# Kernel optimization log

Hardware: AMD Instinct MI355X
Metric: run time of the kernel (lower is better)

Reference implementation:

```python
import jax, jax.numpy as jnp
import numpy as np

B, C, H, W = 2, 128, 48, 48
NUM_HEADS = 8


def dct_matrix(N):
    # Orthonormal DCT-II matrix: D[k, n] = s_k * cos(pi * (n + 0.5) * k / N)
    n = np.arange(N)
    D = np.cos(np.pi * (n[None, :] + 0.5) * n[:, None] / N) * np.sqrt(2.0 / N)
    D[0] *= 1.0 / np.sqrt(2.0)
    return jnp.asarray(D, dtype=jnp.float32)


def setup_inputs() -> dict:
    key = jax.random.key(0)
    ks = jax.random.split(key, 10)
    w_scale = 1.0 / np.sqrt(C)  # kaiming-ish init for 1x1 convs
    inp = {
        "freq_feat": jax.random.normal(ks[0], (B, C, H, W), dtype=jnp.float32),
        "spatial_feat": jax.random.normal(ks[1], (B, C, H, W), dtype=jnp.float32),
        "Wq": jax.random.normal(ks[2], (C, C), dtype=jnp.float32) * w_scale,
        "bq": jnp.zeros((C,), dtype=jnp.float32),
        "Wk": jax.random.normal(ks[3], (C, C), dtype=jnp.float32) * w_scale,
        "bk": jnp.zeros((C,), dtype=jnp.float32),
        "Wv": jax.random.normal(ks[4], (C, C), dtype=jnp.float32) * w_scale,
        "bv": jnp.zeros((C,), dtype=jnp.float32),
        "Wo": jax.random.normal(ks[5], (C, C), dtype=jnp.float32) * w_scale,
        "bo": jnp.zeros((C,), dtype=jnp.float32),
    }
    return inp


def _proj(x, Wm, b):
    # 1x1 conv == channel-mixing GEMM
    return jnp.einsum('oc,bchw->bohw', Wm, x) + b[None, :, None, None]


def reference(freq_feat, spatial_feat, Wq, bq, Wk, bk, Wv, bv, Wo, bo):
    b, c, h, w = freq_feat.shape
    nh = NUM_HEADS
    d = c // nh
    L = h * w

    # 2D orthonormal DCT-II of the spatial features
    DH = dct_matrix(h)
    DW = dct_matrix(w)
    spatial_freq = jnp.einsum('hm,bcmn,wn->bchw', DH, spatial_feat, DW)

    Q = _proj(freq_feat, Wq, bq)
    K = _proj(spatial_freq, Wk, bk)
    V = _proj(spatial_freq, Wv, bv)

    # (B, C, H, W) -> (B, nh, L, d)
    def to_heads(x):
        return x.reshape(b, nh, d, L).transpose(0, 1, 3, 2)

    Qh, Kh, Vh = to_heads(Q), to_heads(K), to_heads(V)

    scale = 1.0 / np.sqrt(d)
    scores = jnp.einsum('bhld,bhsd->bhls', Qh, Kh) * scale  # (B, nh, L, L)
    attn = jax.nn.softmax(scores, axis=-1)
    out = jnp.einsum('bhls,bhsd->bhld', attn, Vh)  # (B, nh, L, d)

    out = out.transpose(0, 1, 3, 2).reshape(b, c, h, w)
    return _proj(out, Wo, bo)
```

## Files before the change

kernel.cpp:

```cpp
#include <hip/hip_runtime.h>
#include <math.h>

#define L_TOT 2304
#define C_TOT 128
#define KSCALE 0.36067376022224085f

#if __has_builtin(__builtin_amdgcn_exp2f)
#define EXP2(x) __builtin_amdgcn_exp2f(x)
#else
#define EXP2(x) __expf(0.69314718055994531f * (x))
#endif

typedef float v4f  __attribute__((ext_vector_type(4)));
typedef __bf16 v8bf __attribute__((ext_vector_type(8)));
typedef __bf16 v4bf __attribute__((ext_vector_type(4)));

#define MFMA_16x16x32_BF16(A, B, C) __builtin_amdgcn_mfma_f32_16x16x32_bf16((A), (B), (C), 0, 0, 0)

__device__ __forceinline__ void async_cp16(const __bf16* g, __bf16* l){
  __builtin_amdgcn_global_load_lds((const __attribute__((address_space(1))) unsigned int*)g,
                                   (__attribute__((address_space(3))) unsigned int*)l,
                                   16, 0, 0);
}

#if __has_builtin(__builtin_amdgcn_permlane32_swap)
__device__ __forceinline__ void pl32swap(unsigned &a, unsigned &b){
  auto r = __builtin_amdgcn_permlane32_swap((int)a, (int)b, false, false);
  a = (unsigned)r[0]; b = (unsigned)r[1];
}
#else
__device__ __forceinline__ void pl32swap(unsigned &a, unsigned &b){
  asm volatile("v_permlane32_swap_b32 %0, %1" : "+v"(a), "+v"(b));
}
#endif
#if __has_builtin(__builtin_amdgcn_permlane16_swap)
__device__ __forceinline__ void pl16swap(unsigned &a, unsigned &b){
  auto r = __builtin_amdgcn_permlane16_swap((int)a, (int)b, false, false);
  a = (unsigned)r[0]; b = (unsigned)r[1];
}
#else
__device__ __forceinline__ void pl16swap(unsigned &a, unsigned &b){
  asm volatile("v_permlane16_swap_b32 %0, %1" : "+v"(a), "+v"(b));
}
#endif

template<int MODE>
__device__ __forceinline__ void mfma_proj(const float* __restrict__ W,
                                          const float* __restrict__ bias,
                                          const float* __restrict__ Xb,
                                          __bf16* __restrict__ Yh,
                                          float scale, float bscale,
                                          int n0, __bf16* Bhi, int tid){
  __bf16* Blo = Bhi + 4352;
  const int wave = tid >> 6, lane = tid & 63, qd = lane >> 4, cn = lane & 15;
  const int m0 = wave * 32;
  v8bf ahi[2][4], alo[2][4];
  #pragma unroll
  for (int rt = 0; rt < 2; rt++)
    #pragma unroll
    for (int ks = 0; ks < 4; ks++){
      const float* wp = W + (size_t)(m0 + rt * 16 + cn) * C_TOT + ks * 32 + qd * 8;
      float4 w0 = *(const float4*)wp;
      float4 w1 = *(const float4*)(wp + 4);
      float wv[8] = {w0.x, w0.y, w0.z, w0.w, w1.x, w1.y, w1.z, w1.w};
      #pragma unroll
      for (int j = 0; j < 8; j++){
        __bf16 h = (__bf16)wv[j];
        ahi[rt][ks][j] = h;
        alo[rt][ks][j] = (__bf16)(wv[j] - (float)h);
      }
    }
  {
    int k = tid >> 1, nh = tid & 1;
    const float* xp = Xb + (size_t)k * L_TOT + n0 + nh * 16;
    float4 x0 = *(const float4*)xp;
    float4 x1 = *(const float4*)(xp + 4);
    float4 x2 = *(const float4*)(xp + 8);
    float4 x3 = *(const float4*)(xp + 12);
    float xv[16] = {x0.x, x0.y, x0.z, x0.w, x1.x, x1.y, x1.z, x1.w,
                    x2.x, x2.y, x2.z, x2.w, x3.x, x3.y, x3.z, x3.w};
    #pragma unroll
    for (int i = 0; i < 16; i++){
      __bf16 h = (__bf16)xv[i];
      int row = nh * 16 + i;
      Bhi[row * 136 + k] = h;
      Blo[row * 136 + k] = (__bf16)(xv[i] - (float)h);
    }
  }
  __syncthreads();
  v4f acc[2][2];
  #pragma unroll
  for (int rt = 0; rt < 2; rt++)
    #pragma unroll
    for (int ct = 0; ct < 2; ct++) acc[rt][ct] = (v4f){0.f, 0.f, 0.f, 0.f};
  #pragma unroll
  for (int ks = 0; ks < 4; ks++){
    v8bf bhi[2], blo[2];
    #pragma unroll
    for (int ct = 0; ct < 2; ct++){
      bhi[ct] = *(const v8bf*)&Bhi[(ct * 16 + cn) * 136 + ks * 32 + qd * 8];
      blo[ct] = *(const v8bf*)&Blo[(ct * 16 + cn) * 136 + ks * 32 + qd * 8];
    }
    #pragma unroll
    for (int rt = 0; rt < 2; rt++)
      #pragma unroll
      for (int ct = 0; ct < 2; ct++){
        acc[rt][ct] = MFMA_16x16x32_BF16(ahi[rt][ks], bhi[ct], acc[rt][ct]);
        acc[rt][ct] = MFMA_16x16x32_BF16(ahi[rt][ks], blo[ct], acc[rt][ct]);
        acc[rt][ct] = MFMA_16x16x32_BF16(alo[rt][ks], bhi[ct], acc[rt][ct]);
      }
  }
  #pragma unroll
  for (int rt = 0; rt < 2; rt++){
    float bv[4];
    #pragma unroll
    for (int r = 0; r < 4; r++) bv[r] = bias[m0 + rt * 16 + qd * 4 + r] * bscale;
    #pragma unroll
    for (int ct = 0; ct < 2; ct++){
      int col = n0 + ct * 16 + cn;
      if (MODE == 1){
        v4bf kk;
        #pragma unroll
        for (int r = 0; r < 4; r++) kk[r] = (__bf16)((acc[rt][ct][r] + bv[r]) * scale);
        *(v4bf*)&Yh[(size_t)col * C_TOT + m0 + rt * 16 + qd * 4] = kk;
      } else {
        #pragma unroll
        for (int r = 0; r < 4; r++)
          Yh[(size_t)(m0 + rt * 16 + qd * 4 + r) * L_TOT + col] = (__bf16)(acc[rt][ct][r] + bv[r]);
      }
    }
  }
}

__global__ __launch_bounds__(256) void k_q_dct(
    const float* __restrict__ freq, const float* __restrict__ spat,
    const float* __restrict__ Wq, const float* __restrict__ bq,
    __bf16* __restrict__ QT, float* __restrict__ SF){
  __shared__ __align__(16) unsigned char smraw[34560];
  int tid = threadIdx.x;
  if (blockIdx.x < 144){
    int idx = blockIdx.x;
    int b = idx / 72, n0 = (idx % 72) * 32;
    size_t off = (size_t)b * C_TOT * L_TOT;
    mfma_proj<1>(Wq, bq, freq + off, QT + (size_t)b * L_TOT * C_TOT, 1.0f, 1.0f, n0, (__bf16*)smraw, tid);
    return;
  }
  int img = blockIdx.x - 144;
  __bf16* Xhi = (__bf16*)smraw;
  __bf16* Xlo = Xhi + 3456;
  __bf16* Dm  = Xhi + 6912;
  __bf16* Thi = Xhi + 10368;
  __bf16* Tlo = Xhi + 13824;
  const float* src = spat + (size_t)img * 2304;
  for (int i = tid; i < 8640; i += 256) ((unsigned int*)smraw)[i] = 0u;
  __syncthreads();
  for (int i = tid; i < 2304; i += 256){
    int a = i / 48, n = i - a * 48;
    int m = ((2 * n + 1) * a) % 192;
    float v = cosf(0.032724923474893679f * (float)m) * 0.204124145231931508f;
    if (a == 0) v *= 0.707106781186547524f;
    Dm[a * 72 + n] = (__bf16)v;
  }
  for (int i = tid; i < 2304; i += 256){
    int mm = i / 48, n = i - mm * 48;
    float v = src[i];
    __bf16 h = (__bf16)v;
    Xhi[mm * 72 + n] = h;
    Xlo[mm * 72 + n] = (__bf16)(v - (float)h);
  }
  __syncthreads();
  int wave = tid >> 6, lane = tid & 63, qd = lane >> 4, cn = lane & 15;
  for (int t = wave; t < 9; t += 4){
    int mi = t / 3, wi = t - mi * 3;
    v8bf ah0 = *(const v8bf*)&Xhi[(mi * 16 + cn) * 72 + qd * 8];
    v8bf ah1 = *(const v8bf*)&Xhi[(mi * 16 + cn) * 72 + 32 + qd * 8];
    v8bf al0 = *(const v8bf*)&Xlo[(mi * 16 + cn) * 72 + qd * 8];
    v8bf al1 = *(const v8bf*)&Xlo[(mi * 16 + cn) * 72 + 32 + qd * 8];
    v8bf b0 = *(const v8bf*)&Dm[(wi * 16 + cn) * 72 + qd * 8];
    v8bf b1 = *(const v8bf*)&Dm[(wi * 16 + cn) * 72 + 32 + qd * 8];
    v4f acc = (v4f){0.f, 0.f, 0.f, 0.f};
    acc = MFMA_16x16x32_BF16(ah0, b0, acc);
    acc = MFMA_16x16x32_BF16(ah1, b1, acc);
    acc = MFMA_16x16x32_BF16(al0, b0, acc);
    acc = MFMA_16x16x32_BF16(al1, b1, acc);
    v4bf th, tl;
    #pragma unroll
    for (int r = 0; r < 4; r++){
      __bf16 h = (__bf16)acc[r];
      th[r] = h;
      tl[r] = (__bf16)(acc[r] - (float)h);
    }
    *(v4bf*)&Thi[(wi * 16 + cn) * 72 + mi * 16 + qd * 4] = th;
    *(v4bf*)&Tlo[(wi * 16 + cn) * 72 + mi * 16 + qd * 4] = tl;
  }
  __syncthreads();
  float* dst = SF + (size_t)img * 2304;
  for (int t = wave; t < 9; t += 4){
    int hi_ = t / 3, wi = t - hi_ * 3;
    v8bf a0 = *(const v8bf*)&Dm[(hi_ * 16 + cn) * 72 + qd * 8];
    v8bf a1 = *(const v8bf*)&Dm[(hi_ * 16 + cn) * 72 + 32 + qd * 8];
    v8bf bh0 = *(const v8bf*)&Thi[(wi * 16 + cn) * 72 + qd * 8];
    v8bf bh1 = *(const v8bf*)&Thi[(wi * 16 + cn) * 72 + 32 + qd * 8];
    v8bf bl0 = *(const v8bf*)&Tlo[(wi * 16 + cn) * 72 + qd * 8];
    v8bf bl1 = *(const v8bf*)&Tlo[(wi * 16 + cn) * 72 + 32 + qd * 8];
    v4f acc = (v4f){0.f, 0.f, 0.f, 0.f};
    acc = MFMA_16x16x32_BF16(a0, bh0, acc);
    acc = MFMA_16x16x32_BF16(a1, bh1, acc);
    acc = MFMA_16x16x32_BF16(a0, bl0, acc);
    acc = MFMA_16x16x32_BF16(a1, bl1, acc);
    int w = wi * 16 + cn;
    #pragma unroll
    for (int r = 0; r < 4; r++)
      dst[(size_t)(hi_ * 16 + qd * 4 + r) * 48 + w] = acc[r];
  }
}

__global__ __launch_bounds__(256) void k_kv(
    const float* __restrict__ SF,
    const float* __restrict__ Wk, const float* __restrict__ bk,
    const float* __restrict__ Wv, const float* __restrict__ bv,
    __bf16* __restrict__ KT, __bf16* __restrict__ Vg){
  __shared__ __align__(16) unsigned char smraw[17408];
  int job = blockIdx.x / 144;
  int idx = blockIdx.x % 144;
  int b = idx / 72, n0 = (idx % 72) * 32;
  size_t off = (size_t)b * C_TOT * L_TOT;
  if (job == 0)
    mfma_proj<1>(Wk, bk, SF + off, KT + (size_t)b * L_TOT * C_TOT, KSCALE, 1.0f, n0, (__bf16*)smraw, threadIdx.x);
  else
    mfma_proj<2>(Wv, bv, SF + off, Vg + off, 1.0f, 1.0f, n0, (__bf16*)smraw, threadIdx.x);
}

__global__ __launch_bounds__(256) void k_attn(const __bf16* __restrict__ QT,
                                              const __bf16* __restrict__ KT,
                                              const __bf16* __restrict__ V,
                                              __bf16* __restrict__ AO){
  const int L = L_TOT;
  int bh = blockIdx.y;
  int b = bh >> 3, h = bh & 7;
  int c0 = h * 16;
  const __bf16* QTb = QT + (size_t)b * L * C_TOT;
  const __bf16* KTb = KT + (size_t)b * L * C_TOT;
  const __bf16* Vb  = V  + ((size_t)b * C_TOT + c0) * L;
  int tid = threadIdx.x;
  int wave = tid >> 6, lane = tid & 63;
  int qd = lane >> 4, cn = lane & 15;
  int l0 = blockIdx.x * 48;

  __shared__ __align__(16) __bf16 smem[8192 + 8192];
  __bf16* Kt = smem;
  __bf16* Vs = smem + 8192;

  v8bf qf[3];
  #pragma unroll
  for (int t = 0; t < 3; t++){
    #pragma unroll
    for (int j = 0; j < 8; j++) qf[t][j] = (__bf16)0.0f;
  }
  if (qd < 2){
    #pragma unroll
    for (int t = 0; t < 3; t++)
      qf[t] = *(const v8bf*)&QTb[(size_t)(l0 + t * 16 + cn) * C_TOT + c0 + qd * 8];
  }

  v4f acc[3];
  float den[3] = {0.f, 0.f, 0.f};
  #pragma unroll
  for (int t = 0; t < 3; t++) acc[t] = (v4f){0.f, 0.f, 0.f, 0.f};

  for (int ch = 0; ch < 5; ch++){
    int s0 = ch * 512;
    int cnt = (ch == 4) ? 256 : 512;
    __syncthreads();
    {
      int per = (cnt >> 5) >> 2;
      for (int jj = 0; jj < per; jj++){
        int j = wave * per + jj;
        int s = j * 32 + (lane >> 1);
        async_cp16(KTb + (size_t)(s0 + s) * C_TOT + c0 + (lane & 1) * 8,
                   Kt + j * 512);
      }
      if (cnt == 512){
        #pragma unroll
        for (int jj = 0; jj < 4; jj++){
          int d = wave * 4 + jj;
          async_cp16(Vb + (size_t)d * L + s0 + ((lane ^ (d & 7)) << 3),
                     Vs + d * 512);
        }
      } else {
        int d = tid >> 4, og = tid & 15;
        const __bf16* gp = Vb + (size_t)d * L + s0 + og * 16;
        v8bf v0 = *(const v8bf*)gp;
        v8bf v1 = *(const v8bf*)(gp + 8);
        int pd = d & 7;
        *(v8bf*)&Vs[d * 512 + (((og * 2)     ^ pd) << 3)] = v0;
        *(v8bf*)&Vs[d * 512 + (((og * 2 + 1) ^ pd) << 3)] = v1;
      }
    }
    __syncthreads();

    int nsu = cnt >> 7;
    int wbase = wave * (cnt >> 2);
    for (int su = 0; su < nsu; su++){
      int sb = wbase + su * 32;
      v8bf a0, a1;
      #pragma unroll
      for (int j = 0; j < 8; j++){ a0[j] = (__bf16)0.0f; a1[j] = (__bf16)0.0f; }
      if (qd < 2){
        a0 = *(const v8bf*)&Kt[(sb + cn) * 16 + qd * 8];
        a1 = *(const v8bf*)&Kt[(sb + 16 + cn) * 16 + qd * 8];
      }
      int jv = sb >> 3;
      v8bf vf = *(const v8bf*)&Vs[cn * 512 + (((jv + qd) ^ (cn & 7)) << 3)];
      #pragma unroll
      for (int t = 0; t < 3; t++){
        v4f z = {0.f, 0.f, 0.f, 0.f};
        v4f st0 = MFMA_16x16x32_BF16(a0, qf[t], z);
        v4f st1 = MFMA_16x16x32_BF16(a1, qf[t], z);
        float p0[4], p1[4];
        #pragma unroll
        for (int i = 0; i < 4; i++){
          p0[i] = EXP2(st0[i]); den[t] += p0[i];
          p1[i] = EXP2(st1[i]); den[t] += p1[i];
        }
        v4bf cc0, cc1;
        #pragma unroll
        for (int i = 0; i < 4; i++){ cc0[i] = (__bf16)p0[i]; cc1[i] = (__bf16)p1[i]; }
        unsigned U0 = ((unsigned*)&cc0)[0], U1 = ((unsigned*)&cc0)[1];
        unsigned U2 = ((unsigned*)&cc1)[0], U3 = ((unsigned*)&cc1)[1];
        pl32swap(U0, U2); pl32swap(U1, U3);
        pl16swap(U0, U2); pl16swap(U1, U3);
        v8bf pf;
        ((unsigned*)&pf)[0] = U0; ((unsigned*)&pf)[1] = U1;
        ((unsigned*)&pf)[2] = U2; ((unsigned*)&pf)[3] = U3;
        acc[t] = MFMA_16x16x32_BF16(vf, pf, acc[t]);
      }
    }
  }

  __syncthreads();
  float* redA = (float*)smem;
  float* redD = (float*)smem + 3072;
  #pragma unroll
  for (int t = 0; t < 3; t++){
    *(v4f*)&redA[((wave * 3 + t) * 64 + lane) * 4] = acc[t];
    redD[(wave * 3 + t) * 64 + lane] = den[t];
  }
  __syncthreads();
  if (wave < 3){
    int t = wave;
    v4f a = (v4f){0.f, 0.f, 0.f, 0.f};
    float dn = 0.f;
    #pragma unroll
    for (int w2 = 0; w2 < 4; w2++){
      v4f xx = *(const v4f*)&redA[((w2 * 3 + t) * 64 + lane) * 4];
      a[0] += xx[0]; a[1] += xx[1]; a[2] += xx[2]; a[3] += xx[3];
      dn += redD[(w2 * 3 + t) * 64 + lane];
    }
    dn += __shfl_xor(dn, 16);
    dn += __shfl_xor(dn, 32);
    float inv = 1.0f / dn;
    __bf16* Ao = AO + ((size_t)b * C_TOT + c0) * L;
    #pragma unroll
    for (int r2 = 0; r2 < 4; r2++)
      Ao[(size_t)(qd * 4 + r2) * L + l0 + t * 16 + cn] = (__bf16)(a[r2] * inv);
  }
}

__global__ __launch_bounds__(256) void k_oproj(const __bf16* __restrict__ AO,
                                               const float* __restrict__ Wo, const float* __restrict__ bo,
                                               float* __restrict__ out){
  __shared__ __align__(16) __bf16 Bs[32 * 136];
  int b = blockIdx.y, n0 = blockIdx.x * 32;
  int tid = threadIdx.x;
  const int wave = tid >> 6, lane = tid & 63, qd = lane >> 4, cn = lane & 15;
  const int m0 = wave * 32;
  v8bf ahi[2][4], alo[2][4];
  #pragma unroll
  for (int rt = 0; rt < 2; rt++)
    #pragma unroll
    for (int ks = 0; ks < 4; ks++){
      const float* wp = Wo + (size_t)(m0 + rt * 16 + cn) * C_TOT + ks * 32 + qd * 8;
      float4 w0 = *(const float4*)wp;
      float4 w1 = *(const float4*)(wp + 4);
      float wv[8] = {w0.x, w0.y, w0.z, w0.w, w1.x, w1.y, w1.z, w1.w};
      #pragma unroll
      for (int j = 0; j < 8; j++){
        __bf16 h = (__bf16)wv[j];
        ahi[rt][ks][j] = h;
        alo[rt][ks][j] = (__bf16)(wv[j] - (float)h);
      }
    }
  {
    int k = tid >> 1, nh = tid & 1;
    const __bf16* src = AO + ((size_t)b * C_TOT + k) * L_TOT + n0 + nh * 16;
    v8bf x0 = *(const v8bf*)src;
    v8bf x1 = *(const v8bf*)(src + 8);
    #pragma unroll
    for (int i = 0; i < 8; i++){
      Bs[(nh * 16 + i) * 136 + k] = x0[i];
      Bs[(nh * 16 + 8 + i) * 136 + k] = x1[i];
    }
  }
  __syncthreads();
  v4f acc[2][2];
  #pragma unroll
  for (int rt = 0; rt < 2; rt++)
    #pragma unroll
    for (int ct = 0; ct < 2; ct++) acc[rt][ct] = (v4f){0.f, 0.f, 0.f, 0.f};
  #pragma unroll
  for (int ks = 0; ks < 4; ks++){
    v8bf bf[2];
    #pragma unroll
    for (int ct = 0; ct < 2; ct++)
      bf[ct] = *(const v8bf*)&Bs[(ct * 16 + cn) * 136 + ks * 32 + qd * 8];
    #pragma unroll
    for (int rt = 0; rt < 2; rt++)
      #pragma unroll
      for (int ct = 0; ct < 2; ct++){
        acc[rt][ct] = MFMA_16x16x32_BF16(ahi[rt][ks], bf[ct], acc[rt][ct]);
        acc[rt][ct] = MFMA_16x16x32_BF16(alo[rt][ks], bf[ct], acc[rt][ct]);
      }
  }
  float* ob = out + (size_t)b * C_TOT * L_TOT;
  #pragma unroll
  for (int rt = 0; rt < 2; rt++){
    float bv[4];
    #pragma unroll
    for (int r = 0; r < 4; r++) bv[r] = bo[m0 + rt * 16 + qd * 4 + r];
    #pragma unroll
    for (int ct = 0; ct < 2; ct++){
      int col = n0 + ct * 16 + cn;
      #pragma unroll
      for (int r = 0; r < 4; r++)
        ob[(size_t)(m0 + rt * 16 + qd * 4 + r) * L_TOT + col] = acc[rt][ct][r] + bv[r];
    }
  }
}

extern "C" void kernel_launch(void* const* d_in, const int* in_sizes, int n_in,
                              void* d_out, int out_size, void* d_ws, size_t ws_size,
                              hipStream_t stream){
  const float* freq = (const float*)d_in[0];
  const float* spat = (const float*)d_in[1];
  const float* Wq = (const float*)d_in[2]; const float* bq = (const float*)d_in[3];
  const float* Wk = (const float*)d_in[4]; const float* bk = (const float*)d_in[5];
  const float* Wv = (const float*)d_in[6]; const float* bv = (const float*)d_in[7];
  const float* Wo = (const float*)d_in[8]; const float* bo = (const float*)d_in[9];
  __bf16* base = (__bf16*)d_ws;

  __bf16* QTg = base;
  __bf16* KTg = base + 589824;
  __bf16* Vg  = base + 1179648;
  __bf16* AOg = base + 1769472;
  float*  SFg = (float*)(base + 2359296);
  float* out = (float*)d_out;

  k_q_dct<<<dim3(400), dim3(256), 0, stream>>>(freq, spat, Wq, bq, QTg, SFg);
  k_kv<<<dim3(288), dim3(256), 0, stream>>>(SFg, Wk, bk, Wv, bv, KTg, Vg);
  k_attn<<<dim3(48, 16), dim3(256), 0, stream>>>(QTg, KTg, Vg, AOg);
  k_oproj<<<dim3(72, 2), dim3(256), 0, stream>>>(AOg, Wo, bo, out);
}
```

Baseline: 115.8 us.

## Double-buffer per-wave K/V async staging in attention and halve projection tiles

The attention kernel replaces its block-wide five-chunk K/V staging loop, which needed two __syncthreads per chunk, with per-wave double-buffered async copies. Each wave prefetches the next 64-key slice while computing on the current one, synchronised only by vmcnt waits, so load latency should overlap with MFMA work. Separately, the Q, K/V and output projection kernels move to 16-column tiles, doubling the block count to fill more CUs at the cost of reloading and splitting the weights more often. The per-wave buffers mean each wave handles only its own key range, and the split-precision weight setup is repeated in twice as many blocks.

```diff
diff --git a/kernel.cpp b/kernel.cpp
--- a/kernel.cpp
+++ b/kernel.cpp
@@ -44,14 +44,14 @@
 }
 #endif
 
-template<int MODE>
+template<int MODE, int NT>
 __device__ __forceinline__ void mfma_proj(const float* __restrict__ W,
                                           const float* __restrict__ bias,
                                           const float* __restrict__ Xb,
                                           __bf16* __restrict__ Yh,
                                           float scale, float bscale,
                                           int n0, __bf16* Bhi, int tid){
-  __bf16* Blo = Bhi + 4352;
+  __bf16* Blo = Bhi + NT * 2176;
   const int wave = tid >> 6, lane = tid & 63, qd = lane >> 4, cn = lane & 15;
   const int m0 = wave * 32;
   v8bf ahi[2][4], alo[2][4];
@@ -70,7 +70,7 @@
         alo[rt][ks][j] = (__bf16)(wv[j] - (float)h);
       }
     }
-  {
+  if (NT == 2){
     int k = tid >> 1, nh = tid & 1;
     const float* xp = Xb + (size_t)k * L_TOT + n0 + nh * 16;
     float4 x0 = *(const float4*)xp;
@@ -86,25 +86,38 @@
       Bhi[row * 136 + k] = h;
       Blo[row * 136 + k] = (__bf16)(xv[i] - (float)h);
     }
-  }
-  __syncthreads();
-  v4f acc[2][2];
+  } else {
+    int k = tid >> 1, half = tid & 1;
+    const float* xp = Xb + (size_t)k * L_TOT + n0 + half * 8;
+    float4 x0 = *(const float4*)xp;
+    float4 x1 = *(const float4*)(xp + 4);
+    float xv[8] = {x0.x, x0.y, x0.z, x0.w, x1.x, x1.y, x1.z, x1.w};
+    #pragma unroll
+    for (int i = 0; i < 8; i++){
+      __bf16 h = (__bf16)xv[i];
+      int row = half * 8 + i;
+      Bhi[row * 136 + k] = h;
+      Blo[row * 136 + k] = (__bf16)(xv[i] - (float)h);
+    }
+  }
+  __syncthreads();
+  v4f acc[2][NT];
   #pragma unroll
   for (int rt = 0; rt < 2; rt++)
     #pragma unroll
-    for (int ct = 0; ct < 2; ct++) acc[rt][ct] = (v4f){0.f, 0.f, 0.f, 0.f};
+    for (int ct = 0; ct < NT; ct++) acc[rt][ct] = (v4f){0.f, 0.f, 0.f, 0.f};
   #pragma unroll
   for (int ks = 0; ks < 4; ks++){
-    v8bf bhi[2], blo[2];
-    #pragma unroll
-    for (int ct = 0; ct < 2; ct++){
+    v8bf bhi[NT], blo[NT];
+    #pragma unroll
+    for (int ct = 0; ct < NT; ct++){
       bhi[ct] = *(const v8bf*)&Bhi[(ct * 16 + cn) * 136 + ks * 32 + qd * 8];
       blo[ct] = *(const v8bf*)&Blo[(ct * 16 + cn) * 136 + ks * 32 + qd * 8];
     }
     #pragma unroll
     for (int rt = 0; rt < 2; rt++)
       #pragma unroll
-      for (int ct = 0; ct < 2; ct++){
+      for (int ct = 0; ct < NT; ct++){
         acc[rt][ct] = MFMA_16x16x32_BF16(ahi[rt][ks], bhi[ct], acc[rt][ct]);
         acc[rt][ct] = MFMA_16x16x32_BF16(ahi[rt][ks], blo[ct], acc[rt][ct]);
         acc[rt][ct] = MFMA_16x16x32_BF16(alo[rt][ks], bhi[ct], acc[rt][ct]);
@@ -116,7 +129,7 @@
     #pragma unroll
     for (int r = 0; r < 4; r++) bv[r] = bias[m0 + rt * 16 + qd * 4 + r] * bscale;
     #pragma unroll
-    for (int ct = 0; ct < 2; ct++){
+    for (int ct = 0; ct < NT; ct++){
       int col = n0 + ct * 16 + cn;
       if (MODE == 1){
         v4bf kk;
@@ -138,14 +151,14 @@
     __bf16* __restrict__ QT, float* __restrict__ SF){
   __shared__ __align__(16) unsigned char smraw[34560];
   int tid = threadIdx.x;
-  if (blockIdx.x < 144){
+  if (blockIdx.x < 288){
     int idx = blockIdx.x;
-    int b = idx / 72, n0 = (idx % 72) * 32;
+    int b = idx / 144, n0 = (idx % 144) * 16;
     size_t off = (size_t)b * C_TOT * L_TOT;
-    mfma_proj<1>(Wq, bq, freq + off, QT + (size_t)b * L_TOT * C_TOT, 1.0f, 1.0f, n0, (__bf16*)smraw, tid);
+    mfma_proj<1, 1>(Wq, bq, freq + off, QT + (size_t)b * L_TOT * C_TOT, 1.0f, 1.0f, n0, (__bf16*)smraw, tid);
     return;
   }
-  int img = blockIdx.x - 144;
+  int img = blockIdx.x - 288;
   __bf16* Xhi = (__bf16*)smraw;
   __bf16* Xlo = Xhi + 3456;
   __bf16* Dm  = Xhi + 6912;
@@ -220,15 +233,15 @@
     const float* __restrict__ Wk, const float* __restrict__ bk,
     const float* __restrict__ Wv, const float* __restrict__ bv,
     __bf16* __restrict__ KT, __bf16* __restrict__ Vg){
-  __shared__ __align__(16) unsigned char smraw[17408];
-  int job = blockIdx.x / 144;
-  int idx = blockIdx.x % 144;
-  int b = idx / 72, n0 = (idx % 72) * 32;
+  __shared__ __align__(16) unsigned char smraw[8704];
+  int job = blockIdx.x / 288;
+  int idx = blockIdx.x % 288;
+  int b = idx / 144, n0 = (idx % 144) * 16;
   size_t off = (size_t)b * C_TOT * L_TOT;
   if (job == 0)
-    mfma_proj<1>(Wk, bk, SF + off, KT + (size_t)b * L_TOT * C_TOT, KSCALE, 1.0f, n0, (__bf16*)smraw, threadIdx.x);
+    mfma_proj<1, 1>(Wk, bk, SF + off, KT + (size_t)b * L_TOT * C_TOT, KSCALE, 1.0f, n0, (__bf16*)smraw, threadIdx.x);
   else
-    mfma_proj<2>(Wv, bv, SF + off, Vg + off, 1.0f, 1.0f, n0, (__bf16*)smraw, threadIdx.x);
+    mfma_proj<2, 1>(Wv, bv, SF + off, Vg + off, 1.0f, 1.0f, n0, (__bf16*)smraw, threadIdx.x);
 }
 
 __global__ __launch_bounds__(256) void k_attn(const __bf16* __restrict__ QT,
@@ -247,9 +260,9 @@
   int qd = lane >> 4, cn = lane & 15;
   int l0 = blockIdx.x * 48;
 
-  __shared__ __align__(16) __bf16 smem[8192 + 8192];
-  __bf16* Kt = smem;
-  __bf16* Vs = smem + 8192;
+  __shared__ __align__(16) __bf16 smem[16384];
+  __bf16* KtW = smem + wave * 2048;
+  __bf16* VsW = smem + 8192 + wave * 2048;
 
   v8bf qf[3];
   #pragma unroll
@@ -268,50 +281,45 @@
   #pragma unroll
   for (int t = 0; t < 3; t++) acc[t] = (v4f){0.f, 0.f, 0.f, 0.f};
 
-  for (int ch = 0; ch < 5; ch++){
-    int s0 = ch * 512;
-    int cnt = (ch == 4) ? 256 : 512;
-    __syncthreads();
-    {
-      int per = (cnt >> 5) >> 2;
-      for (int jj = 0; jj < per; jj++){
-        int j = wave * per + jj;
-        int s = j * 32 + (lane >> 1);
-        async_cp16(KTb + (size_t)(s0 + s) * C_TOT + c0 + (lane & 1) * 8,
-                   Kt + j * 512);
-      }
-      if (cnt == 512){
-        #pragma unroll
-        for (int jj = 0; jj < 4; jj++){
-          int d = wave * 4 + jj;
-          async_cp16(Vb + (size_t)d * L + s0 + ((lane ^ (d & 7)) << 3),
-                     Vs + d * 512);
-        }
-      } else {
-        int d = tid >> 4, og = tid & 15;
-        const __bf16* gp = Vb + (size_t)d * L + s0 + og * 16;
-        v8bf v0 = *(const v8bf*)gp;
-        v8bf v1 = *(const v8bf*)(gp + 8);
-        int pd = d & 7;
-        *(v8bf*)&Vs[d * 512 + (((og * 2)     ^ pd) << 3)] = v0;
-        *(v8bf*)&Vs[d * 512 + (((og * 2 + 1) ^ pd) << 3)] = v1;
-      }
-    }
-    __syncthreads();
-
-    int nsu = cnt >> 7;
-    int wbase = wave * (cnt >> 2);
-    for (int su = 0; su < nsu; su++){
-      int sb = wbase + su * 32;
+  #define STAGE4(CH, BUF)                                                          \
+    {                                                                              \
+      int s0w = (CH) * 256 + wave * 64;                                            \
+      _Pragma("unroll")                                                            \
+      for (int j = 0; j < 2; j++)                                                  \
+        async_cp16(KTb + (size_t)(s0w + j * 32 + (lane >> 1)) * C_TOT + c0 +       \
+                       (lane & 1) * 8,                                             \
+                   KtW + (BUF) * 1024 + j * 512);                                  \
+      _Pragma("unroll")                                                            \
+      for (int j = 0; j < 2; j++)                                                  \
+        async_cp16(Vb + (size_t)(j * 8 + (lane >> 3)) * L + s0w +                  \
+                       (((lane & 7) ^ ((lane >> 3) & 7)) << 3),                    \
+                   VsW + (BUF) * 1024 + j * 512);                                  \
+    }
+
+  STAGE4(0, 0);
+
+  for (int ch = 0; ch < 9; ch++){
+    int p = ch & 1;
+    if (ch < 8){
+      STAGE4(ch + 1, p ^ 1);
+      asm volatile("s_waitcnt vmcnt(4)" ::: "memory");
+    } else {
+      asm volatile("s_waitcnt vmcnt(0)" ::: "memory");
+    }
+    __builtin_amdgcn_sched_barrier(0);
+
+    const __bf16* Kt = KtW + p * 1024;
+    const __bf16* Vs = VsW + p * 1024;
+    #pragma unroll
+    for (int su = 0; su < 2; su++){
       v8bf a0, a1;
       #pragma unroll
       for (int j = 0; j < 8; j++){ a0[j] = (__bf16)0.0f; a1[j] = (__bf16)0.0f; }
       if (qd < 2){
-        a0 = *(const v8bf*)&Kt[(sb + cn) * 16 + qd * 8];
-        a1 = *(const v8bf*)&Kt[(sb + 16 + cn) * 16 + qd * 8];
-      }
-      int jv = sb >> 3;
-      v8bf vf = *(const v8bf*)&Vs[cn * 512 + (((jv + qd) ^ (cn & 7)) << 3)];
+        a0 = *(const v8bf*)&Kt[(su * 32 + cn) * 16 + qd * 8];
+        a1 = *(const v8bf*)&Kt[(su * 32 + 16 + cn) * 16 + qd * 8];
+      }
+      v8bf vf = *(const v8bf*)&Vs[cn * 64 + (((su * 32 + qd * 8)) ^ ((cn & 7) << 3))];
       #pragma unroll
       for (int t = 0; t < 3; t++){
         v4f z = {0.f, 0.f, 0.f, 0.f};
@@ -337,6 +345,7 @@
       }
     }
   }
+  #undef STAGE4
 
   __syncthreads();
   float* redA = (float*)smem;
@@ -370,8 +379,8 @@
 __global__ __launch_bounds__(256) void k_oproj(const __bf16* __restrict__ AO,
                                                const float* __restrict__ Wo, const float* __restrict__ bo,
                                                float* __restrict__ out){
-  __shared__ __align__(16) __bf16 Bs[32 * 136];
-  int b = blockIdx.y, n0 = blockIdx.x * 32;
+  __shared__ __align__(16) __bf16 Bs[16 * 136];
+  int b = blockIdx.y, n0 = blockIdx.x * 16;
   int tid = threadIdx.x;
   const int wave = tid >> 6, lane = tid & 63, qd = lane >> 4, cn = lane & 15;
   const int m0 = wave * 32;
@@ -392,35 +401,25 @@
       }
     }
   {
-    int k = tid >> 1, nh = tid & 1;
-    const __bf16* src = AO + ((size_t)b * C_TOT + k) * L_TOT + n0 + nh * 16;
+    int k = tid >> 1, half = tid & 1;
+    const __bf16* src = AO + ((size_t)b * C_TOT + k) * L_TOT + n0 + half * 8;
     v8bf x0 = *(const v8bf*)src;
-    v8bf x1 = *(const v8bf*)(src + 8);
-    #pragma unroll
-    for (int i = 0; i < 8; i++){
-      Bs[(nh * 16 + i) * 136 + k] = x0[i];
-      Bs[(nh * 16 + 8 + i) * 136 + k] = x1[i];
-    }
-  }
-  __syncthreads();
-  v4f acc[2][2];
-  #pragma unroll
-  for (int rt = 0; rt < 2; rt++)
-    #pragma unroll
-    for (int ct = 0; ct < 2; ct++) acc[rt][ct] = (v4f){0.f, 0.f, 0.f, 0.f};
+    #pragma unroll
+    for (int i = 0; i < 8; i++)
+      Bs[(half * 8 + i) * 136 + k] = x0[i];
+  }
+  __syncthreads();
+  v4f acc[2];
+  #pragma unroll
+  for (int rt = 0; rt < 2; rt++) acc[rt] = (v4f){0.f, 0.f, 0.f, 0.f};
   #pragma unroll
   for (int ks = 0; ks < 4; ks++){
-    v8bf bf[2];
-    #pragma unroll
-    for (int ct = 0; ct < 2; ct++)
-      bf[ct] = *(const v8bf*)&Bs[(ct * 16 + cn) * 136 + ks * 32 + qd * 8];
-    #pragma unroll
-    for (int rt = 0; rt < 2; rt++)
-      #pragma unroll
-      for (int ct = 0; ct < 2; ct++){
-        acc[rt][ct] = MFMA_16x16x32_BF16(ahi[rt][ks], bf[ct], acc[rt][ct]);
-        acc[rt][ct] = MFMA_16x16x32_BF16(alo[rt][ks], bf[ct], acc[rt][ct]);
-      }
+    v8bf bf = *(const v8bf*)&Bs[cn * 136 + ks * 32 + qd * 8];
+    #pragma unroll
+    for (int rt = 0; rt < 2; rt++){
+      acc[rt] = MFMA_16x16x32_BF16(ahi[rt][ks], bf, acc[rt]);
+      acc[rt] = MFMA_16x16x32_BF16(alo[rt][ks], bf, acc[rt]);
+    }
   }
   float* ob = out + (size_t)b * C_TOT * L_TOT;
   #pragma unroll
@@ -428,13 +427,10 @@
     float bv[4];
     #pragma unroll
     for (int r = 0; r < 4; r++) bv[r] = bo[m0 + rt * 16 + qd * 4 + r];
-    #pragma unroll
-    for (int ct = 0; ct < 2; ct++){
-      int col = n0 + ct * 16 + cn;
-      #pragma unroll
-      for (int r = 0; r < 4; r++)
-        ob[(size_t)(m0 + rt * 16 + qd * 4 + r) * L_TOT + col] = acc[rt][ct][r] + bv[r];
-    }
+    int col = n0 + cn;
+    #pragma unroll
+    for (int r = 0; r < 4; r++)
+      ob[(size_t)(m0 + rt * 16 + qd * 4 + r) * L_TOT + col] = acc[rt][r] + bv[r];
   }
 }
 
@@ -456,8 +452,8 @@
   float*  SFg = (float*)(base + 2359296);
   float* out = (float*)d_out;
 
-  k_q_dct<<<dim3(400), dim3(256), 0, stream>>>(freq, spat, Wq, bq, QTg, SFg);
-  k_kv<<<dim3(288), dim3(256), 0, stream>>>(SFg, Wk, bk, Wv, bv, KTg, Vg);
+  k_q_dct<<<dim3(544), dim3(256), 0, stream>>>(freq, spat, Wq, bq, QTg, SFg);
+  k_kv<<<dim3(576), dim3(256), 0, stream>>>(SFg, Wk, bk, Wv, bv, KTg, Vg);
   k_attn<<<dim3(48, 16), dim3(256), 0, stream>>>(QTg, KTg, Vg, AOg);
-  k_oproj<<<dim3(72, 2), dim3(256), 0, stream>>>(AOg, Wo, bo, out);
-}
+  k_oproj<<<dim3(144, 2), dim3(256), 0, stream>>>(AOg, Wo, bo, out);
+}
```

New measurement: 116.5 us. No clear change (+0.7%).

## Double-buffer per-wave K tiles and register-prefetch V in attention kernel

Applied to the files above, without the earlier changes.

The attention kernel moves to 512 threads (8 waves), each owning a private double-buffered LDS slot for its K sub-tile. The next tile's K is loaded asynchronously and V is prefetched straight into registers while the current tile is computed, with vmcnt waits in place of block-wide barriers and the shared V staging. A two-stage cross-wave reduction combines the extra waves' partial sums. The aim is to hide global-load latency, remove the per-chunk __syncthreads, and raise occupancy, at the cost of uncoalesced per-lane V loads and a longer reduction epilogue.

```diff
diff --git a/kernel.cpp b/kernel.cpp
--- a/kernel.cpp
+++ b/kernel.cpp
@@ -231,7 +231,55 @@
     mfma_proj<2>(Wv, bv, SF + off, Vg + off, 1.0f, 1.0f, n0, (__bf16*)smraw, threadIdx.x);
 }
 
-__global__ __launch_bounds__(256) void k_attn(const __bf16* __restrict__ QT,
+__device__ __forceinline__ void attn_step(
+    int ch, int prefetch, __bf16* KtW, const __bf16* KTb, const __bf16* Vb,
+    int c0, int wave, int lane, int qd, int cn,
+    const v8bf (&qf)[3], const v8bf& vUse, v8bf& vNext,
+    v4f (&acc)[3], float (&den)[3]){
+  if (prefetch){
+    int s0n = (ch + 1) * 256 + wave * 32;
+    async_cp16(KTb + (size_t)(s0n + (lane >> 1)) * C_TOT + c0 + (lane & 1) * 8,
+               KtW + (((ch + 1) & 1) << 9) + lane * 8);
+    vNext = *(const v8bf*)(Vb + (size_t)cn * L_TOT + (ch + 1) * 256 + wave * 32 + qd * 8);
+    asm volatile("s_waitcnt vmcnt(2)" ::: "memory");
+  } else {
+    asm volatile("s_waitcnt vmcnt(0)" ::: "memory");
+  }
+  __builtin_amdgcn_sched_barrier(0);
+  const __bf16* Kt = KtW + ((ch & 1) << 9);
+  v8bf a0, a1;
+  #pragma unroll
+  for (int j = 0; j < 8; j++){ a0[j] = (__bf16)0.0f; a1[j] = (__bf16)0.0f; }
+  if (qd < 2){
+    a0 = *(const v8bf*)&Kt[cn * 16 + qd * 8];
+    a1 = *(const v8bf*)&Kt[(16 + cn) * 16 + qd * 8];
+  }
+  #pragma unroll
+  for (int t = 0; t < 3; t++){
+    v4f z = {0.f, 0.f, 0.f, 0.f};
+    v4f st0 = MFMA_16x16x32_BF16(a0, qf[t], z);
+    v4f st1 = MFMA_16x16x32_BF16(a1, qf[t], z);
+    float p0[4], p1[4];
+    #pragma unroll
+    for (int i = 0; i < 4; i++){
+      p0[i] = EXP2(st0[i]); den[t] += p0[i];
+      p1[i] = EXP2(st1[i]); den[t] += p1[i];
+    }
+    v4bf cc0, cc1;
+    #pragma unroll
+    for (int i = 0; i < 4; i++){ cc0[i] = (__bf16)p0[i]; cc1[i] = (__bf16)p1[i]; }
+    unsigned U0 = ((unsigned*)&cc0)[0], U1 = ((unsigned*)&cc0)[1];
+    unsigned U2 = ((unsigned*)&cc1)[0], U3 = ((unsigned*)&cc1)[1];
+    pl32swap(U0, U2); pl32swap(U1, U3);
+    pl16swap(U0, U2); pl16swap(U1, U3);
+    v8bf pf;
+    ((unsigned*)&pf)[0] = U0; ((unsigned*)&pf)[1] = U1;
+    ((unsigned*)&pf)[2] = U2; ((unsigned*)&pf)[3] = U3;
+    acc[t] = MFMA_16x16x32_BF16(vUse, pf, acc[t]);
+  }
+}
+
+__global__ __launch_bounds__(512) void k_attn(const __bf16* __restrict__ QT,
                                               const __bf16* __restrict__ KT,
                                               const __bf16* __restrict__ V,
                                               __bf16* __restrict__ AO){
@@ -247,9 +295,8 @@
   int qd = lane >> 4, cn = lane & 15;
   int l0 = blockIdx.x * 48;
 
-  __shared__ __align__(16) __bf16 smem[8192 + 8192];
-  __bf16* Kt = smem;
-  __bf16* Vs = smem + 8192;
+  __shared__ __align__(16) __bf16 smem[8192];
+  __bf16* KtW = smem + wave * 1024;
 
   v8bf qf[3];
   #pragma unroll
@@ -268,83 +315,43 @@
   #pragma unroll
   for (int t = 0; t < 3; t++) acc[t] = (v4f){0.f, 0.f, 0.f, 0.f};
 
-  for (int ch = 0; ch < 5; ch++){
-    int s0 = ch * 512;
-    int cnt = (ch == 4) ? 256 : 512;
-    __syncthreads();
-    {
-      int per = (cnt >> 5) >> 2;
-      for (int jj = 0; jj < per; jj++){
-        int j = wave * per + jj;
-        int s = j * 32 + (lane >> 1);
-        async_cp16(KTb + (size_t)(s0 + s) * C_TOT + c0 + (lane & 1) * 8,
-                   Kt + j * 512);
-      }
-      if (cnt == 512){
-        #pragma unroll
-        for (int jj = 0; jj < 4; jj++){
-          int d = wave * 4 + jj;
-          async_cp16(Vb + (size_t)d * L + s0 + ((lane ^ (d & 7)) << 3),
-                     Vs + d * 512);
-        }
-      } else {
-        int d = tid >> 4, og = tid & 15;
-        const __bf16* gp = Vb + (size_t)d * L + s0 + og * 16;
-        v8bf v0 = *(const v8bf*)gp;
-        v8bf v1 = *(const v8bf*)(gp + 8);
-        int pd = d & 7;
-        *(v8bf*)&Vs[d * 512 + (((og * 2)     ^ pd) << 3)] = v0;
-        *(v8bf*)&Vs[d * 512 + (((og * 2 + 1) ^ pd) << 3)] = v1;
-      }
-    }
-    __syncthreads();
-
-    int nsu = cnt >> 7;
-    int wbase = wave * (cnt >> 2);
-    for (int su = 0; su < nsu; su++){
-      int sb = wbase + su * 32;
-      v8bf a0, a1;
-      #pragma unroll
-      for (int j = 0; j < 8; j++){ a0[j] = (__bf16)0.0f; a1[j] = (__bf16)0.0f; }
-      if (qd < 2){
-        a0 = *(const v8bf*)&Kt[(sb + cn) * 16 + qd * 8];
-        a1 = *(const v8bf*)&Kt[(sb + 16 + cn) * 16 + qd * 8];
-      }
-      int jv = sb >> 3;
-      v8bf vf = *(const v8bf*)&Vs[cn * 512 + (((jv + qd) ^ (cn & 7)) << 3)];
-      #pragma unroll
-      for (int t = 0; t < 3; t++){
-        v4f z = {0.f, 0.f, 0.f, 0.f};
-        v4f st0 = MFMA_16x16x32_BF16(a0, qf[t], z);
-        v4f st1 = MFMA_16x16x32_BF16(a1, qf[t], z);
-        float p0[4], p1[4];
-        #pragma unroll
-        for (int i = 0; i < 4; i++){
-          p0[i] = EXP2(st0[i]); den[t] += p0[i];
-          p1[i] = EXP2(st1[i]); den[t] += p1[i];
-        }
-        v4bf cc0, cc1;
-        #pragma unroll
-        for (int i = 0; i < 4; i++){ cc0[i] = (__bf16)p0[i]; cc1[i] = (__bf16)p1[i]; }
-        unsigned U0 = ((unsigned*)&cc0)[0], U1 = ((unsigned*)&cc0)[1];
-        unsigned U2 = ((unsigned*)&cc1)[0], U3 = ((unsigned*)&cc1)[1];
-        pl32swap(U0, U2); pl32swap(U1, U3);
-        pl16swap(U0, U2); pl16swap(U1, U3);
-        v8bf pf;
-        ((unsigned*)&pf)[0] = U0; ((unsigned*)&pf)[1] = U1;
-        ((unsigned*)&pf)[2] = U2; ((unsigned*)&pf)[3] = U3;
-        acc[t] = MFMA_16x16x32_BF16(vf, pf, acc[t]);
-      }
-    }
-  }
+  v8bf vA, vB;
+  async_cp16(KTb + (size_t)(wave * 32 + (lane >> 1)) * C_TOT + c0 + (lane & 1) * 8,
+             KtW + lane * 8);
+  vA = *(const v8bf*)(Vb + (size_t)cn * L + wave * 32 + qd * 8);
+
+  for (int cc = 0; cc < 4; cc++){
+    attn_step(2 * cc,     1, KtW, KTb, Vb, c0, wave, lane, qd, cn, qf, vA, vB, acc, den);
+    attn_step(2 * cc + 1, 1, KtW, KTb, Vb, c0, wave, lane, qd, cn, qf, vB, vA, acc, den);
+  }
+  attn_step(8, 0, KtW, KTb, Vb, c0, wave, lane, qd, cn, qf, vA, vB, acc, den);
 
   __syncthreads();
   float* redA = (float*)smem;
   float* redD = (float*)smem + 3072;
-  #pragma unroll
-  for (int t = 0; t < 3; t++){
-    *(v4f*)&redA[((wave * 3 + t) * 64 + lane) * 4] = acc[t];
-    redD[(wave * 3 + t) * 64 + lane] = den[t];
+  if (wave >= 4){
+    #pragma unroll
+    for (int t = 0; t < 3; t++){
+      *(v4f*)&redA[(((wave - 4) * 3 + t) * 64 + lane) * 4] = acc[t];
+      redD[((wave - 4) * 3 + t) * 64 + lane] = den[t];
+    }
+  }
+  __syncthreads();
+  if (wave < 4){
+    #pragma unroll
+    for (int t = 0; t < 3; t++){
+      v4f xx = *(const v4f*)&redA[((wave * 3 + t) * 64 + lane) * 4];
+      acc[t][0] += xx[0]; acc[t][1] += xx[1]; acc[t][2] += xx[2]; acc[t][3] += xx[3];
+      den[t] += redD[(wave * 3 + t) * 64 + lane];
+    }
+  }
+  __syncthreads();
+  if (wave < 4){
+    #pragma unroll
+    for (int t = 0; t < 3; t++){
+      *(v4f*)&redA[((wave * 3 + t) * 64 + lane) * 4] = acc[t];
+      redD[(wave * 3 + t) * 64 + lane] = den[t];
+    }
   }
   __syncthreads();
   if (wave < 3){
@@ -458,6 +465,6 @@
 
   k_q_dct<<<dim3(400), dim3(256), 0, stream>>>(freq, spat, Wq, bq, QTg, SFg);
   k_kv<<<dim3(288), dim3(256), 0, stream>>>(SFg, Wk, bk, Wv, bv, KTg, Vg);
-  k_attn<<<dim3(48, 16), dim3(256), 0, stream>>>(QTg, KTg, Vg, AOg);
+  k_attn<<<dim3(48, 16), dim3(512), 0, stream>>>(QTg, KTg, Vg, AOg);
   k_oproj<<<dim3(72, 2), dim3(256), 0, stream>>>(AOg, Wo, bo, out);
 }
```

New measurement: 113.0 us. 1.02x faster.
